# Performance work log

Hardware: AMD Instinct MI355X
Metric: run time of the kernel (lower is better)

The kernel has to match this reference:

```python
import jax, jax.numpy as jnp
import numpy as np
import math

EMBED = 1024
HEADS = 16
HEAD_DIM = EMBED // HEADS
B, S = 2, 2048


def setup_inputs() -> dict:
    key = jax.random.key(0)
    ks = jax.random.split(key, 12)
    sc = 1.0 / math.sqrt(EMBED)
    inp = {
        'query': jax.random.normal(ks[0], (B, S, EMBED), jnp.float32),
        'key': jax.random.normal(ks[1], (B, S, EMBED), jnp.float32),
        'values': jax.random.normal(ks[2], (B, S, EMBED), jnp.float32),
        # causal mask, broadcastable to [B, H, S, S]; masked where == 0
        'mask': jnp.tril(jnp.ones((S, S), jnp.int32))[None, None, :, :],
        'Wq': jax.random.normal(ks[3], (EMBED, EMBED), jnp.float32) * sc,
        'bq': jnp.zeros((EMBED,), jnp.float32),
        'Wk': jax.random.normal(ks[4], (EMBED, EMBED), jnp.float32) * sc,
        'bk': jnp.zeros((EMBED,), jnp.float32),
        'Wv': jax.random.normal(ks[5], (EMBED, EMBED), jnp.float32) * sc,
        'bv': jnp.zeros((EMBED,), jnp.float32),
        'Wo': jax.random.normal(ks[6], (EMBED, EMBED), jnp.float32) * sc,
        'bo': jnp.zeros((EMBED,), jnp.float32),
    }
    return inp


def reference(query, key, values, mask, Wq, bq, Wk, bk, Wv, bv, Wo, bo):
    # linear projections (torch Linear: x @ W.T + b)
    q = query @ Wq.T + bq
    k = key @ Wk.T + bk
    v = values @ Wv.T + bv
    b, sq, _ = q.shape
    sk = k.shape[1]
    q = q.reshape(b, sq, HEADS, HEAD_DIM)  # bqhd
    k = k.reshape(b, sk, HEADS, HEAD_DIM)  # bkhd
    v = v.reshape(b, sk, HEADS, HEAD_DIM)  # bkhd
    energy = jnp.einsum('bqhd,bkhd->bhqk', q, k) / math.sqrt(HEAD_DIM)
    energy = jnp.where(mask == 0, jnp.float32(-1e10), energy)
    attn = jax.nn.softmax(energy, axis=-1)
    out = jnp.einsum('bhqk,bkhd->bqhd', attn, v).reshape(b, sq, EMBED)
    return out @ Wo.T + bo
```

## Files before the change

### kernel.cpp

```cpp
#include <hip/hip_runtime.h>

typedef unsigned short u16;
typedef unsigned int   u32;
typedef __attribute__((ext_vector_type(4)))  float f32x4;
typedef __attribute__((ext_vector_type(8)))  short bf16x8;
typedef __attribute__((ext_vector_type(4)))  u32   u32x4;
typedef __attribute__((ext_vector_type(4)))  u16   u16x4;

#define AS1 __attribute__((address_space(1)))
#define AS3 __attribute__((address_space(3)))

__device__ __forceinline__ u16 f2bf(float f) {
  union { float f; u32 u; } v; v.f = f;
  u32 r = v.u + 0x7FFFu + ((v.u >> 16) & 1u);
  return (u16)(r >> 16);
}

__device__ __forceinline__ u16 f2bf_t(float f) {
  union { float f; u32 u; } v; v.f = f;
  return (u16)(v.u >> 16);
}

__device__ __forceinline__ void g2l16(const void* g, void* l) {
  __builtin_amdgcn_global_load_lds((const AS1 u32*)g, (AS3 u32*)l, 16, 0, 0);
}

struct CvtArgs {
  const float* src[7];
  u16*         dst[7];
  int          n4[7];
};

__global__ __launch_bounds__(256) void cvt_kernel(CvtArgs a) {
  const int ai = blockIdx.y;
  const f32x4* s = (const f32x4*)a.src[ai];
  u16x4*       d = (u16x4*)a.dst[ai];
  const int n4 = a.n4[ai];
  for (int i = blockIdx.x * 256 + threadIdx.x; i < n4; i += gridDim.x * 256) {
    f32x4 v = s[i];
    u16x4 o;
    o[0] = f2bf(v[0]); o[1] = f2bf(v[1]); o[2] = f2bf(v[2]); o[3] = f2bf(v[3]);
    d[i] = o;
  }
}

template <typename OutT, int TM>
__device__ __forceinline__ void gemm_core64(
    const u16* __restrict__ A, const u16* __restrict__ W,
    const float* __restrict__ bias, bool rowbias, float oscale,
    OutT* __restrict__ C, int ldc, int row0, int col0,
    u16* sA, u16* sB, int tid)
{
  constexpr int K = 1024;
  constexpr int MF = TM / 32;
  const int lane = tid & 63, wid = tid >> 6;
  const int l15 = lane & 15, hi = lane >> 4;
  const int wr = (wid >> 1) * (TM / 2), wc = (wid & 1) * 64;

  f32x4 acc[MF][4];
#pragma unroll
  for (int i = 0; i < MF; ++i)
#pragma unroll
    for (int j = 0; j < 4; ++j) acc[i][j] = f32x4{0.f, 0.f, 0.f, 0.f};

  auto stage = [&](int kt) {
#pragma unroll
    for (int it = 0; it < TM / 32; ++it) {
      int idx = it * 256 + tid;
      int r = idx >> 3, g = idx & 7;
      int gs = g ^ (r & 7);
      g2l16(A + (size_t)(row0 + r) * K + kt * 64 + gs * 8, sA + idx * 8);
    }
#pragma unroll
    for (int it = 0; it < 4; ++it) {
      int idx = it * 256 + tid;
      int r = idx >> 3, g = idx & 7;
      int gs = g ^ (r & 7);
      g2l16(W + (size_t)(col0 + r) * K + kt * 64 + gs * 8, sB + idx * 8);
    }
  };

  stage(0);
  for (int kt = 0; kt < K / 64; ++kt) {
    __syncthreads();
    bf16x8 aF[MF][2], bF[4][2];
#pragma unroll
    for (int mf = 0; mf < MF; ++mf) {
      int r = wr + mf * 16 + l15;
#pragma unroll
      for (int kh = 0; kh < 2; ++kh)
        aF[mf][kh] = *(const bf16x8*)(sA + r * 64 + ((kh * 4 + hi) ^ (r & 7)) * 8);
    }
#pragma unroll
    for (int nf = 0; nf < 4; ++nf) {
      int r = wc + nf * 16 + l15;
#pragma unroll
      for (int kh = 0; kh < 2; ++kh)
        bF[nf][kh] = *(const bf16x8*)(sB + r * 64 + ((kh * 4 + hi) ^ (r & 7)) * 8);
    }
    __syncthreads();
    if (kt + 1 < K / 64) stage(kt + 1);
#pragma unroll
    for (int kh = 0; kh < 2; ++kh)
#pragma unroll
      for (int mf = 0; mf < MF; ++mf)
#pragma unroll
        for (int nf = 0; nf < 4; ++nf)
          acc[mf][nf] = __builtin_amdgcn_mfma_f32_16x16x32_bf16(aF[mf][kh], bF[nf][kh], acc[mf][nf], 0, 0, 0);
  }

#pragma unroll
  for (int nf = 0; nf < 4; ++nf) {
    int gcol = col0 + wc + nf * 16 + l15;
    float bcol = rowbias ? 0.f : bias[gcol];
#pragma unroll
    for (int mf = 0; mf < MF; ++mf) {
#pragma unroll
      for (int r = 0; r < 4; ++r) {
        int grow = row0 + wr + mf * 16 + hi * 4 + r;
        float bv = rowbias ? bias[grow] : bcol;
        float v = (acc[mf][nf][r] + bv) * oscale;
        if constexpr (sizeof(OutT) == 2) {
          ((u16*)C)[(size_t)grow * ldc + gcol] = f2bf(v);
        } else {
          ((float*)C)[(size_t)grow * ldc + gcol] = v;
        }
      }
    }
  }
}

struct ProjArgs {
  const u16* A[3]; const u16* W[3]; const float* bias[3];
  u16* C[3];
  float scale[3];
};

__global__ __launch_bounds__(256, 2) void gemm_proj(ProjArgs p) {
  __shared__ alignas(16) u16 sA[128 * 64];
  __shared__ alignas(16) u16 sB[128 * 64];
  const int w = (blockIdx.x & 7) * 96 + (blockIdx.x >> 3);
  int which, row0, col0, ldc;
  bool rowbias;
  if (w < 512) {
    which = w >> 8;
    int l = w & 255;
    col0 = (l & 7) << 7;
    row0 = (l >> 3) << 7;
    ldc = 1024; rowbias = false;
  } else {
    which = 2;
    int l = w - 512;
    col0 = (l & 31) << 7;
    row0 = (l >> 5) << 7;
    ldc = 4096; rowbias = true;
  }
  gemm_core64<u16, 128>(p.A[which], p.W[which], p.bias[which], rowbias,
                        p.scale[which],
                        p.C[which], ldc, row0, col0, sA, sB, threadIdx.x);
}

__global__ __launch_bounds__(256, 2) void gemm_out(
    const u16* __restrict__ A, const u16* __restrict__ W,
    const float* __restrict__ bias, float* __restrict__ C)
{
  __shared__ alignas(16) u16 sA[64 * 64];
  __shared__ alignas(16) u16 sB[128 * 64];
  const int w = (blockIdx.x & 7) * 64 + (blockIdx.x >> 3);
  const int col0 = (w & 7) << 7;
  const int row0 = (w >> 3) << 6;
  gemm_core64<float, 64>(A, W, bias, false, 1.0f, C, 1024, row0, col0,
                         sA, sB, threadIdx.x);
}

__global__ __launch_bounds__(256, 4) void attn_fwd(
    const u16* __restrict__ Q, const u16* __restrict__ Kg, const u16* __restrict__ VT,
    u16* __restrict__ ctx)
{
  __shared__ alignas(16) u16 sK[2][64 * 64];
  __shared__ alignas(16) u16 sVt[2][64 * 64];
  __shared__ alignas(16) u16 sP[4][16 * 64];

  const int tid = threadIdx.x;
  const int lane = tid & 63, wid = tid >> 6;
  const int l15 = lane & 15, hi = lane >> 4;

  const int wg = blockIdx.x;
  const int jj = wg >> 5, bh = wg & 31;
  const int rr = jj >> 3, kk = jj & 7;
  int xt;
  if (rr == 0)      xt = 31 - kk;
  else if (rr == 1) xt = 16 + kk;
  else if (rr == 2) xt = 15 - kk;
  else              xt = kk;

  const int b = bh >> 4, h = bh & 15;
  const int q0 = xt * 64;
  const int q0w = q0 + wid * 16;
  const size_t base  = ((size_t)b * 2048) * 1024 + h * 64;
  const size_t vbase = (size_t)(h * 64) * 4096 + b * 2048;

  bf16x8 qf[2];
#pragma unroll
  for (int kh = 0; kh < 2; ++kh)
    qf[kh] = *(const bf16x8*)(Q + base + (size_t)(q0w + l15) * 1024 + kh * 32 + hi * 8);

  f32x4 o[4];
  float lS = 0.f;
#pragma unroll
  for (int nf = 0; nf < 4; ++nf) o[nf] = f32x4{0.f, 0.f, 0.f, 0.f};

  u16* sPw = &sP[wid][0];
  const int nt = xt + 1;

  auto issueK = [&](int ti, int bb) {
#pragma unroll
    for (int it = 0; it < 2; ++it) {
      int idx = it * 256 + tid;
      int r = idx >> 3, g = idx & 7;
      int gs = g ^ (r & 7);
      g2l16(Kg + base + (size_t)(ti * 64 + r) * 1024 + gs * 8, &sK[bb][idx * 8]);
    }
  };
  auto issueV = [&](int ti, int bb) {
#pragma unroll
    for (int it = 0; it < 2; ++it) {
      int idx = it * 256 + tid;
      int r = idx >> 3, g = idx & 7;
      int gs = g ^ (r & 7);
      g2l16(VT + vbase + (size_t)r * 4096 + ti * 64 + gs * 8, &sVt[bb][idx * 8]);
    }
  };

  issueK(0, 0);
  issueV(0, 0);
  __syncthreads();

  for (int ti = 0; ti < nt; ++ti) {
    const int cur = ti & 1;
    const bool pf = (ti + 1 < nt);
    if (pf) {
      issueK(ti + 1, cur ^ 1);
      issueV(ti + 1, cur ^ 1);
    }

    const int kv0 = ti * 64;
    const bool needmask = (ti == xt);
    const u16* sKc = &sK[cur][0];
    const u16* sVc = &sVt[cur][0];

    f32x4 s[4];
#pragma unroll
    for (int n = 0; n < 4; ++n) s[n] = f32x4{0.f, 0.f, 0.f, 0.f};
#pragma unroll
    for (int n = 0; n < 4; ++n) {
      int kvr = n * 16 + l15;
      bf16x8 kf0 = *(const bf16x8*)(sKc + kvr * 64 + ((hi) ^ (kvr & 7)) * 8);
      bf16x8 kf1 = *(const bf16x8*)(sKc + kvr * 64 + ((4 + hi) ^ (kvr & 7)) * 8);
      s[n] = __builtin_amdgcn_mfma_f32_16x16x32_bf16(kf0, qf[0], s[n], 0, 0, 0);
      s[n] = __builtin_amdgcn_mfma_f32_16x16x32_bf16(kf1, qf[1], s[n], 0, 0, 0);
    }

#pragma unroll
    for (int n = 0; n < 4; ++n) {
      int kabase = kv0 + n * 16 + hi * 4;
      int qa = q0w + l15;
#pragma unroll
      for (int r = 0; r < 4; ++r) {
        float sv = s[n][r];
        if (needmask && (kabase + r > qa)) sv = -1e30f;
        float p = __builtin_amdgcn_exp2f(sv);
        s[n][r] = p;
        lS += p;
      }
    }

#pragma unroll
    for (int n = 0; n < 4; ++n) {
      u16x4 pk;
      pk[0] = f2bf_t(s[n][0]); pk[1] = f2bf_t(s[n][1]);
      pk[2] = f2bf_t(s[n][2]); pk[3] = f2bf_t(s[n][3]);
      int kvb = n * 16 + hi * 4;
      *(u16x4*)(sPw + l15 * 64 + (kvb ^ ((l15 & 7) << 3))) = pk;
    }

#pragma unroll
    for (int kq = 0; kq < 2; ++kq) {
      bf16x8 pa, vb[4];
      pa = *(const bf16x8*)(sPw + l15 * 64 + ((kq * 32 + hi * 8) ^ ((l15 & 7) << 3)));
#pragma unroll
      for (int nf = 0; nf < 4; ++nf) {
        int rd = nf * 16 + l15;
        vb[nf] = *(const bf16x8*)(sVc + rd * 64 + ((kq * 4 + hi) ^ (rd & 7)) * 8);
      }
#pragma unroll
      for (int nf = 0; nf < 4; ++nf)
        o[nf] = __builtin_amdgcn_mfma_f32_16x16x32_bf16(pa, vb[nf], o[nf], 0, 0, 0);
    }

    __syncthreads();
  }

  float t = lS;
  t += __shfl_xor(t, 16);
  t += __shfl_xor(t, 32);
#pragma unroll
  for (int r = 0; r < 4; ++r) {
    float lr = __shfl(t, hi * 4 + r);
    float inv = 1.f / lr;
    size_t rowoff = base + (size_t)(q0w + hi * 4 + r) * 1024;
#pragma unroll
    for (int nf = 0; nf < 4; ++nf)
      ctx[rowoff + nf * 16 + l15] = f2bf(o[nf][r] * inv);
  }
}

extern "C" void kernel_launch(void* const* d_in, const int* in_sizes, int n_in,
                              void* d_out, int out_size, void* d_ws, size_t ws_size,
                              hipStream_t stream) {
  const float* query = (const float*)d_in[0];
  const float* key   = (const float*)d_in[1];
  const float* vals  = (const float*)d_in[2];
  const float* Wq = (const float*)d_in[4];
  const float* bq = (const float*)d_in[5];
  const float* Wk = (const float*)d_in[6];
  const float* bk = (const float*)d_in[7];
  const float* Wv = (const float*)d_in[8];
  const float* bv = (const float*)d_in[9];
  const float* Wo = (const float*)d_in[10];
  const float* bo = (const float*)d_in[11];
  float* out = (float*)d_out;

  if (ws_size < 58720256) return;

  u16* ws = (u16*)d_ws;
  u16* xq = ws + 0;
  u16* xk = ws + 4194304;
  u16* xv = ws + 8388608;
  u16* wq = ws + 12582912;
  u16* wk = ws + 13631488;
  u16* wv = ws + 14680064;
  u16* wo = ws + 15728640;
  u16* Qb = ws + 16777216;
  u16* Kb = ws + 20971520;
  u16* VT = ws + 25165824;
  u16* ctx = xq;

  CvtArgs ca;
  ca.src[0] = query; ca.dst[0] = xq; ca.n4[0] = 1048576;
  ca.src[1] = key;   ca.dst[1] = xk; ca.n4[1] = 1048576;
  ca.src[2] = vals;  ca.dst[2] = xv; ca.n4[2] = 1048576;
  ca.src[3] = Wq;    ca.dst[3] = wq; ca.n4[3] = 262144;
  ca.src[4] = Wk;    ca.dst[4] = wk; ca.n4[4] = 262144;
  ca.src[5] = Wv;    ca.dst[5] = wv; ca.n4[5] = 262144;
  ca.src[6] = Wo;    ca.dst[6] = wo; ca.n4[6] = 262144;
  cvt_kernel<<<dim3(256, 7), 256, 0, stream>>>(ca);

  constexpr float SCL = 0.125f * 1.44269504f;
  ProjArgs pa;
  pa.A[0] = xq; pa.W[0] = wq; pa.bias[0] = bq; pa.C[0] = Qb; pa.scale[0] = SCL;
  pa.A[1] = xk; pa.W[1] = wk; pa.bias[1] = bk; pa.C[1] = Kb; pa.scale[1] = 1.0f;
  pa.A[2] = wv; pa.W[2] = xv; pa.bias[2] = bv; pa.C[2] = VT; pa.scale[2] = 1.0f;
  gemm_proj<<<dim3(768), 256, 0, stream>>>(pa);

  attn_fwd<<<dim3(1024), 256, 0, stream>>>(Qb, Kb, VT, ctx);

  gemm_out<<<dim3(512), 256, 0, stream>>>(ctx, wo, bo, out);
}
```

Before: 106.6 us.

## Double-buffer GEMM LDS tiles with K-step 32 to overlap loads and MFMA

```diff
diff --git a/kernel.cpp b/kernel.cpp
--- a/kernel.cpp
+++ b/kernel.cpp
@@ -45,7 +45,7 @@
 }
 
 template <typename OutT, int TM>
-__device__ __forceinline__ void gemm_core64(
+__device__ __forceinline__ void gemm_core32(
     const u16* __restrict__ A, const u16* __restrict__ W,
     const float* __restrict__ bias, bool rowbias, float oscale,
     OutT* __restrict__ C, int ldc, int row0, int col0,
@@ -63,50 +63,48 @@
 #pragma unroll
     for (int j = 0; j < 4; ++j) acc[i][j] = f32x4{0.f, 0.f, 0.f, 0.f};
 
-  auto stage = [&](int kt) {
-#pragma unroll
-    for (int it = 0; it < TM / 32; ++it) {
+  auto stage = [&](int kt, int bb) {
+    u16* dA = sA + bb * (TM * 32);
+    u16* dB = sB + bb * (128 * 32);
+#pragma unroll
+    for (int it = 0; it < TM / 64; ++it) {
       int idx = it * 256 + tid;
-      int r = idx >> 3, g = idx & 7;
-      int gs = g ^ (r & 7);
-      g2l16(A + (size_t)(row0 + r) * K + kt * 64 + gs * 8, sA + idx * 8);
-    }
-#pragma unroll
-    for (int it = 0; it < 4; ++it) {
+      int r = idx >> 2, g = idx & 3;
+      int gs = g ^ ((r >> 1) & 3);
+      g2l16(A + (size_t)(row0 + r) * K + kt * 32 + gs * 8, dA + idx * 8);
+    }
+#pragma unroll
+    for (int it = 0; it < 2; ++it) {
       int idx = it * 256 + tid;
-      int r = idx >> 3, g = idx & 7;
-      int gs = g ^ (r & 7);
-      g2l16(W + (size_t)(col0 + r) * K + kt * 64 + gs * 8, sB + idx * 8);
+      int r = idx >> 2, g = idx & 3;
+      int gs = g ^ ((r >> 1) & 3);
+      g2l16(W + (size_t)(col0 + r) * K + kt * 32 + gs * 8, dB + idx * 8);
     }
   };
 
-  stage(0);
-  for (int kt = 0; kt < K / 64; ++kt) {
+  stage(0, 0);
+  for (int kt = 0; kt < K / 32; ++kt) {
     __syncthreads();
-    bf16x8 aF[MF][2], bF[4][2];
+    const int cur = kt & 1;
+    if (kt + 1 < K / 32) stage(kt + 1, cur ^ 1);
+    const u16* cA = sA + cur * (TM * 32);
+    const u16* cB = sB + cur * (128 * 32);
+    bf16x8 aF[MF], bF[4];
 #pragma unroll
     for (int mf = 0; mf < MF; ++mf) {
       int r = wr + mf * 16 + l15;
-#pragma unroll
-      for (int kh = 0; kh < 2; ++kh)
-        aF[mf][kh] = *(const bf16x8*)(sA + r * 64 + ((kh * 4 + hi) ^ (r & 7)) * 8);
+      aF[mf] = *(const bf16x8*)(cA + r * 32 + (hi ^ ((r >> 1) & 3)) * 8);
     }
 #pragma unroll
     for (int nf = 0; nf < 4; ++nf) {
       int r = wc + nf * 16 + l15;
-#pragma unroll
-      for (int kh = 0; kh < 2; ++kh)
-        bF[nf][kh] = *(const bf16x8*)(sB + r * 64 + ((kh * 4 + hi) ^ (r & 7)) * 8);
-    }
-    __syncthreads();
-    if (kt + 1 < K / 64) stage(kt + 1);
-#pragma unroll
-    for (int kh = 0; kh < 2; ++kh)
-#pragma unroll
-      for (int mf = 0; mf < MF; ++mf)
-#pragma unroll
-        for (int nf = 0; nf < 4; ++nf)
-          acc[mf][nf] = __builtin_amdgcn_mfma_f32_16x16x32_bf16(aF[mf][kh], bF[nf][kh], acc[mf][nf], 0, 0, 0);
+      bF[nf] = *(const bf16x8*)(cB + r * 32 + (hi ^ ((r >> 1) & 3)) * 8);
+    }
+#pragma unroll
+    for (int mf = 0; mf < MF; ++mf)
+#pragma unroll
+      for (int nf = 0; nf < 4; ++nf)
+        acc[mf][nf] = __builtin_amdgcn_mfma_f32_16x16x32_bf16(aF[mf], bF[nf], acc[mf][nf], 0, 0, 0);
   }
 
 #pragma unroll
@@ -137,8 +135,8 @@
 };
 
 __global__ __launch_bounds__(256, 2) void gemm_proj(ProjArgs p) {
-  __shared__ alignas(16) u16 sA[128 * 64];
-  __shared__ alignas(16) u16 sB[128 * 64];
+  __shared__ alignas(16) u16 sA[2 * 128 * 32];
+  __shared__ alignas(16) u16 sB[2 * 128 * 32];
   const int w = (blockIdx.x & 7) * 96 + (blockIdx.x >> 3);
   int which, row0, col0, ldc;
   bool rowbias;
@@ -155,7 +153,7 @@
     row0 = (l >> 5) << 7;
     ldc = 4096; rowbias = true;
   }
-  gemm_core64<u16, 128>(p.A[which], p.W[which], p.bias[which], rowbias,
+  gemm_core32<u16, 128>(p.A[which], p.W[which], p.bias[which], rowbias,
                         p.scale[which],
                         p.C[which], ldc, row0, col0, sA, sB, threadIdx.x);
 }
@@ -164,12 +162,12 @@
     const u16* __restrict__ A, const u16* __restrict__ W,
     const float* __restrict__ bias, float* __restrict__ C)
 {
-  __shared__ alignas(16) u16 sA[64 * 64];
-  __shared__ alignas(16) u16 sB[128 * 64];
+  __shared__ alignas(16) u16 sA[2 * 64 * 32];
+  __shared__ alignas(16) u16 sB[2 * 128 * 32];
   const int w = (blockIdx.x & 7) * 64 + (blockIdx.x >> 3);
   const int col0 = (w & 7) << 7;
   const int row0 = (w >> 3) << 6;
-  gemm_core64<float, 64>(A, W, bias, false, 1.0f, C, 1024, row0, col0,
+  gemm_core32<float, 64>(A, W, bias, false, 1.0f, C, 1024, row0, col0,
                          sA, sB, threadIdx.x);
 }
 
```

Result: slower. 114.1 us (+7.1%).
